# Optimization experiments

Hardware: AMD Instinct MI355X
Metric: run time of the kernel (lower is better)

The kernel has to match this reference:

```python
import jax, jax.numpy as jnp
import numpy as np

D_K = 128
SCALER = np.sqrt(D_K).astype(np.float32)

def setup_inputs() -> dict:
    key = jax.random.key(0)
    kq, kk, kv = jax.random.split(key, 3)
    B, L, D = 16, 2048, D_K
    q = jax.random.normal(kq, (B, L, D), dtype=jnp.float32)
    k = jax.random.normal(kk, (B, L, D), dtype=jnp.float32)
    v = jax.random.normal(kv, (B, L, D), dtype=jnp.float32)
    return {"q": q, "k": k, "v": v}

def reference(q, k, v):
    # score[b, i, j] = q[b, i, :] . k[b, j, :] / sqrt(d_k)
    score = jnp.einsum('bid,bjd->bij', q, k) / SCALER
    attn = jax.nn.softmax(score, axis=-1)
    # output[b, i, :] = sum_j attn[b, i, j] * v[b, j, :]
    return jnp.einsum('bij,bjd->bid', attn, v)
```

## Files before the change

kernel.cpp:

```cpp
#include <hip/hip_runtime.h>
#include <stdint.h>


typedef short bf16x8 __attribute__((ext_vector_type(8)));
typedef float f32x4 __attribute__((ext_vector_type(4)));
typedef float f32x16 __attribute__((ext_vector_type(16)));
typedef unsigned int u32;
typedef unsigned short u16;

#define L_SEQ  2048
#define D_HEAD 128
#define TSZ    8388608u
#define W_PART (2u * TSZ)
#define W_LSUM (W_PART + 768u * 32768u)
#define WS_NEED (W_LSUM + 768u * 128u * 4u)

__device__ __forceinline__ unsigned pk2(float lo, float hi) {
    union { float f; unsigned u; } a, b;
    a.f = lo; b.f = hi;
    return __builtin_amdgcn_perm(b.u + 0x8000u, a.u + 0x8000u, 0x07060302u);
}
__device__ __forceinline__ float ex2(float x) { return __builtin_amdgcn_exp2f(x); }
__device__ __forceinline__ float bflo(unsigned w) {
    union { unsigned u; float f; } v; v.u = w << 16; return v.f;
}
__device__ __forceinline__ float bfhi(unsigned w) {
    union { unsigned u; float f; } v; v.u = w & 0xffff0000u; return v.f;
}
__device__ __forceinline__ u32 cvtpk(float lo, float hi) {
    u32 d;
    asm("v_cvt_pk_bf16_f32 %0, %1, %2" : "=v"(d) : "v"(lo), "v"(hi));
    return d;
}
__device__ __forceinline__ void plswap(u32& a, u32& b) {
    asm volatile("v_permlane32_swap_b32 %0, %1" : "+v"(a), "+v"(b));
}
__device__ __forceinline__ void gl_lds16(const u16* g, u16* l) {
    __builtin_amdgcn_global_load_lds(
        (const __attribute__((address_space(1))) u32*)g,
        (__attribute__((address_space(3))) u32*)l, 16, 0, 0);
}

__global__ __launch_bounds__(256, 4)
void prepass(const float* __restrict__ K, const float* __restrict__ V,
             u16* __restrict__ kb, u16* __restrict__ vt) {
    const int id = blockIdx.x, t = threadIdx.x;
    if (id < 512) {
        const float* src = K + (size_t)id * 64 * 128;
        u16*        dst = kb + (size_t)id * 64 * 128;
        const int r = t >> 2;
        #pragma unroll
        for (int i = 0; i < 4; ++i) {
            int gp = (t & 3) * 4 + i;
            const float* s = src + r * 128 + gp * 8;
            float4 x0 = *(const float4*)s, x1 = *(const float4*)(s + 4);
            uint4 w;
            w.x = pk2(x0.x, x0.y); w.y = pk2(x0.z, x0.w);
            w.z = pk2(x1.x, x1.y); w.w = pk2(x1.z, x1.w);
            *(uint4*)(dst + (gp * 64 + r) * 8) = w;
        }
    } else {
        __shared__ __align__(16) u16 vl[128 * 72];
        const int bid = id - 512;
        const float* src = V + (size_t)bid * 64 * 128;
        const int vcc = t & 31, vgk = t >> 5;
        union { float4 v; float f[4]; } vr[8];
        const float* vp = src + (size_t)(vgk * 8) * 128 + vcc * 4;
        #pragma unroll
        for (int r = 0; r < 8; ++r) vr[r].v = *(const float4*)(vp + (size_t)r * 128);
        #pragma unroll
        for (int dd = 0; dd < 4; ++dd) {
            uint4 w;
            w.x = pk2(vr[0].f[dd], vr[1].f[dd]);
            w.y = pk2(vr[2].f[dd], vr[3].f[dd]);
            w.z = pk2(vr[4].f[dd], vr[5].f[dd]);
            w.w = pk2(vr[6].f[dd], vr[7].f[dd]);
            *(uint4*)(&vl[(vcc * 4 + dd) * 72 + vgk * 8]) = w;
        }
        __syncthreads();
        u16* dst = vt + (size_t)bid * 8192;
        #pragma unroll
        for (int i = 0; i < 4; ++i) {
            int c = i * 256 + t;
            int gv = c >> 7, d = c & 127;
            uint4 w = *(const uint4*)(&vl[d * 72 + gv * 8]);
            *(uint4*)(dst + (size_t)c * 8) = w;
        }
    }
}

__global__ __launch_bounds__(256, 2)
void attnR(const float* __restrict__ Qg, const u16* __restrict__ kb,
           const u16* __restrict__ vt, u16* __restrict__ part,
           float* __restrict__ lsum) {
    __shared__ __align__(16) char smem[32768];
    const int tid = threadIdx.x;
    const int qs = tid >> 6, lane = tid & 63;
    const int q32 = lane & 31, hi = lane >> 5;
    const int bid = blockIdx.x;
    const int kvh = bid >> 8, p = bid & 255;
    const int b = p & 15, qblk = p >> 4;
    const int t0 = kvh * 11;
    const int nt = (kvh < 2) ? 11 : 10;

    const float* Qp = Qg + (size_t)b * L_SEQ * D_HEAD;
    const u16*   Kp = kb + (size_t)b * L_SEQ * D_HEAD + (size_t)t0 * 8192;
    const u16*   Vp = vt + (size_t)b * 32 * 8192 + (size_t)t0 * 8192;
    u16* Kl = (u16*)smem;
    u16* Vl = (u16*)(smem + 16384);
    const int so = qs * 2048 + lane * 8;

    #pragma unroll
    for (int i = 0; i < 4; ++i) {
        gl_lds16(Kp + so + i * 512, Kl + so + i * 512);
        gl_lds16(Vp + so + i * 512, Vl + so + i * 512);
    }

    const float QS = 1.4426950408889634f / 11.313708498984761f;
    bf16x8 qf[8];
    {
        const float* qrow = Qp + (size_t)(qblk * 128 + qs * 32 + q32) * 128 + hi * 8;
        #pragma unroll
        for (int s8 = 0; s8 < 8; ++s8) {
            float4 x0 = *(const float4*)(qrow + s8 * 16);
            float4 x1 = *(const float4*)(qrow + s8 * 16 + 4);
            union { u32 u[4]; bf16x8 v; } tt;
            tt.u[0] = pk2(x0.x * QS, x0.y * QS);
            tt.u[1] = pk2(x0.z * QS, x0.w * QS);
            tt.u[2] = pk2(x1.x * QS, x1.y * QS);
            tt.u[3] = pk2(x1.z * QS, x1.w * QS);
            qf[s8] = tt.v;
        }
    }

    f32x16 acc[4];
    #pragma unroll
    for (int dt = 0; dt < 4; ++dt)
        acc[dt] = (f32x16){0.f,0.f,0.f,0.f,0.f,0.f,0.f,0.f,
                           0.f,0.f,0.f,0.f,0.f,0.f,0.f,0.f};
    float lrun = 0.f;

    __syncthreads();

    for (int it = 0; it < nt; ++it) {
        f32x16 st0 = (f32x16){0.f,0.f,0.f,0.f,0.f,0.f,0.f,0.f,
                              0.f,0.f,0.f,0.f,0.f,0.f,0.f,0.f};
        f32x16 st1 = st0;
        const u16* Kbase = Kl + hi * 512 + q32 * 8;
        #pragma unroll
        for (int s8 = 0; s8 < 8; ++s8) {
            bf16x8 a0 = *(const bf16x8*)(Kbase + s8 * 1024);
            bf16x8 a1 = *(const bf16x8*)(Kbase + s8 * 1024 + 256);
            st0 = __builtin_amdgcn_mfma_f32_32x32x16_bf16(a0, qf[s8], st0, 0, 0, 0);
            st1 = __builtin_amdgcn_mfma_f32_32x32x16_bf16(a1, qf[s8], st1, 0, 0, 0);
        }
        __syncthreads();

        if (it + 1 < nt) {
            const u16* kg = Kp + (size_t)(it + 1) * 8192 + so;
            #pragma unroll
            for (int i = 0; i < 4; ++i) gl_lds16(kg + i * 512, Kl + so + i * 512);
        }

        bf16x8 pf[4];
        #pragma unroll
        for (int v = 0; v < 2; ++v) {
            float pp[16];
            #pragma unroll
            for (int e = 0; e < 16; ++e) {
                float sv = (v == 0) ? st0[e] : st1[e];
                pp[e] = ex2(sv);
                lrun += pp[e];
            }
            u32 wa0 = cvtpk(pp[0], pp[1]),  wb0 = cvtpk(pp[4], pp[5]);
            u32 wa1 = cvtpk(pp[2], pp[3]),  wb1 = cvtpk(pp[6], pp[7]);
            plswap(wa0, wb0); plswap(wa1, wb1);
            u32 wc0 = cvtpk(pp[8], pp[9]),  wd0 = cvtpk(pp[12], pp[13]);
            u32 wc1 = cvtpk(pp[10], pp[11]), wd1 = cvtpk(pp[14], pp[15]);
            plswap(wc0, wd0); plswap(wc1, wd1);
            union { u32 u[4]; bf16x8 x; } t0u, t1u;
            t0u.u[0] = wa0; t0u.u[1] = wa1; t0u.u[2] = wb0; t0u.u[3] = wb1;
            t1u.u[0] = wc0; t1u.u[1] = wc1; t1u.u[2] = wd0; t1u.u[3] = wd1;
            pf[v * 2]     = t0u.x;
            pf[v * 2 + 1] = t1u.x;
        }

        const u16* Vbase = Vl + hi * 1024 + q32 * 8;
        #pragma unroll
        for (int dt = 0; dt < 4; ++dt) {
            #pragma unroll
            for (int ks = 0; ks < 4; ++ks) {
                bf16x8 av = *(const bf16x8*)(Vbase + ks * 2048 + dt * 256);
                acc[dt] = __builtin_amdgcn_mfma_f32_32x32x16_bf16(av, pf[ks], acc[dt], 0, 0, 0);
            }
        }
        __syncthreads();

        if (it + 1 < nt) {
            const u16* vg = Vp + (size_t)(it + 1) * 8192 + so;
            #pragma unroll
            for (int i = 0; i < 4; ++i) gl_lds16(vg + i * 512, Vl + so + i * 512);
        }
    }

    float l = lrun + __shfl_xor(lrun, 32);
    uint2* pw = (uint2*)(part + (size_t)bid * 16384);
    #pragma unroll
    for (int dt = 0; dt < 4; ++dt) {
        f32x16 o = acc[dt];
        #pragma unroll
        for (int jj = 0; jj < 4; ++jj) {
            uint2 w;
            w.x = pk2(o[jj * 4 + 0], o[jj * 4 + 1]);
            w.y = pk2(o[jj * 4 + 2], o[jj * 4 + 3]);
            pw[(((qs * 4 + dt) * 4 + jj) << 6) + lane] = w;
        }
    }
    if (lane < 32)
        lsum[(size_t)bid * 128 + qs * 32 + lane] = l;
}

__global__ __launch_bounds__(256, 2)
void combineR(const u16* __restrict__ part, const float* __restrict__ lsum,
              float* __restrict__ Og) {
    __shared__ float inv[128];
    __shared__ __align__(16) float Ol[64 * 132];
    const int t = threadIdx.x, p = blockIdx.x;
    const int b = p & 15, qblk = p >> 4;
    if (t < 128) {
        float l = lsum[(size_t)p * 128 + t]
                + lsum[(size_t)(256 + p) * 128 + t]
                + lsum[(size_t)(512 + p) * 128 + t];
        inv[t] = 1.0f / l;
    }
    const uint2* S0 = (const uint2*)(part + (size_t)p * 16384);
    const uint2* S1 = (const uint2*)(part + (size_t)(256 + p) * 16384);
    const uint2* S2 = (const uint2*)(part + (size_t)(512 + p) * 16384);
    __syncthreads();
    #pragma unroll
    for (int h = 0; h < 2; ++h) {
        #pragma unroll
        for (int i = 0; i < 8; ++i) {
            int slot = i * 256 + t;
            int qs_l = slot >> 10;
            int dt   = (slot >> 8) & 3;
            int jj   = (slot >> 6) & 3;
            int lane = slot & 63;
            int hi = lane >> 5, q32 = lane & 31;
            int qs = h * 2 + qs_l;
            int row_l = qs_l * 32 + q32;
            int d0 = dt * 32 + hi * 4 + jj * 8;
            size_t idx = (size_t)(((qs * 4 + dt) * 4 + jj) << 6) + lane;
            uint2 w0 = S0[idx], w1 = S1[idx], w2 = S2[idx];
            float iv = inv[h * 64 + row_l];
            float4 o;
            o.x = (bflo(w0.x) + bflo(w1.x) + bflo(w2.x)) * iv;
            o.y = (bfhi(w0.x) + bfhi(w1.x) + bfhi(w2.x)) * iv;
            o.z = (bflo(w0.y) + bflo(w1.y) + bflo(w2.y)) * iv;
            o.w = (bfhi(w0.y) + bfhi(w1.y) + bfhi(w2.y)) * iv;
            *(float4*)(&Ol[row_l * 132 + d0]) = o;
        }
        __syncthreads();
        #pragma unroll
        for (int i = 0; i < 8; ++i) {
            int slot = i * 256 + t;
            int row = slot >> 5, c4 = slot & 31;
            float4 val = *(const float4*)(&Ol[row * 132 + c4 * 4]);
            size_t q = (size_t)b * L_SEQ + qblk * 128 + h * 64 + row;
            *(float4*)(Og + q * D_HEAD + c4 * 4) = val;
        }
        __syncthreads();
    }
}

extern "C" void kernel_launch(void* const* d_in, const int* in_sizes, int n_in,
                              void* d_out, int out_size, void* d_ws, size_t ws_size,
                              hipStream_t stream) {
    const float* q = (const float*)d_in[0];
    const float* k = (const float*)d_in[1];
    const float* v = (const float*)d_in[2];
    float* out = (float*)d_out;
    u16* kb = (u16*)d_ws;
    u16* vt = (u16*)((char*)d_ws + TSZ);
    u16* part = (u16*)((char*)d_ws + W_PART);
    float* ls = (float*)((char*)d_ws + W_LSUM);
    prepass<<<dim3(1024), dim3(256), 0, stream>>>(k, v, kb, vt);
    attnR<<<dim3(768), dim3(256), 0, stream>>>(q, kb, vt, part, ls);
    combineR<<<dim3(256), dim3(256), 0, stream>>>(part, ls, out);
}
```

Before: 136.8 us.

## Drop split-KV partials and combine pass; each block handles full KV for 64 rows

The attention kernel no longer splits the key sequence into three chunks with bf16 partial outputs and a separate combine kernel. Each block of 128 threads now processes 64 query rows across all 32 KV tiles and writes normalized fp32 output directly. This removes the partial-write traffic, the combine launch and bf16 rounding of partials. In exchange there are fewer and longer blocks (512 blocks of 2 waves), and each block loads K/V tiles from global memory for only 64 rows, so there is less reuse per load and less overlap from waves sharing a tile.

Result: slower. 148.1 us (+8.3%).

```diff
diff --git a/kernel.cpp b/kernel.cpp
--- a/kernel.cpp
+++ b/kernel.cpp
@@ -3,7 +3,6 @@
 
 
 typedef short bf16x8 __attribute__((ext_vector_type(8)));
-typedef float f32x4 __attribute__((ext_vector_type(4)));
 typedef float f32x16 __attribute__((ext_vector_type(16)));
 typedef unsigned int u32;
 typedef unsigned short u16;
@@ -11,9 +10,6 @@
 #define L_SEQ  2048
 #define D_HEAD 128
 #define TSZ    8388608u
-#define W_PART (2u * TSZ)
-#define W_LSUM (W_PART + 768u * 32768u)
-#define WS_NEED (W_LSUM + 768u * 128u * 4u)
 
 __device__ __forceinline__ unsigned pk2(float lo, float hi) {
     union { float f; unsigned u; } a, b;
@@ -21,12 +17,6 @@
     return __builtin_amdgcn_perm(b.u + 0x8000u, a.u + 0x8000u, 0x07060302u);
 }
 __device__ __forceinline__ float ex2(float x) { return __builtin_amdgcn_exp2f(x); }
-__device__ __forceinline__ float bflo(unsigned w) {
-    union { unsigned u; float f; } v; v.u = w << 16; return v.f;
-}
-__device__ __forceinline__ float bfhi(unsigned w) {
-    union { unsigned u; float f; } v; v.u = w & 0xffff0000u; return v.f;
-}
 __device__ __forceinline__ u32 cvtpk(float lo, float hi) {
     u32 d;
     asm("v_cvt_pk_bf16_f32 %0, %1, %2" : "=v"(d) : "v"(lo), "v"(hi));
@@ -89,37 +79,34 @@
     }
 }
 
-__global__ __launch_bounds__(256, 2)
-void attnR(const float* __restrict__ Qg, const u16* __restrict__ kb,
-           const u16* __restrict__ vt, u16* __restrict__ part,
-           float* __restrict__ lsum) {
+__global__ __launch_bounds__(128, 2)
+void attnF(const float* __restrict__ Qg, const u16* __restrict__ kb,
+           const u16* __restrict__ vt, float* __restrict__ Og) {
     __shared__ __align__(16) char smem[32768];
     const int tid = threadIdx.x;
     const int qs = tid >> 6, lane = tid & 63;
     const int q32 = lane & 31, hi = lane >> 5;
-    const int bid = blockIdx.x;
-    const int kvh = bid >> 8, p = bid & 255;
+    const int p = blockIdx.x;
     const int b = p & 15, qblk = p >> 4;
-    const int t0 = kvh * 11;
-    const int nt = (kvh < 2) ? 11 : 10;
+    const int nt = 32;
 
     const float* Qp = Qg + (size_t)b * L_SEQ * D_HEAD;
-    const u16*   Kp = kb + (size_t)b * L_SEQ * D_HEAD + (size_t)t0 * 8192;
-    const u16*   Vp = vt + (size_t)b * 32 * 8192 + (size_t)t0 * 8192;
+    const u16*   Kp = kb + (size_t)b * L_SEQ * D_HEAD;
+    const u16*   Vp = vt + (size_t)b * 32 * 8192;
     u16* Kl = (u16*)smem;
     u16* Vl = (u16*)(smem + 16384);
-    const int so = qs * 2048 + lane * 8;
+    const int so = tid * 8;
 
     #pragma unroll
-    for (int i = 0; i < 4; ++i) {
-        gl_lds16(Kp + so + i * 512, Kl + so + i * 512);
-        gl_lds16(Vp + so + i * 512, Vl + so + i * 512);
+    for (int i = 0; i < 8; ++i) {
+        gl_lds16(Kp + so + i * 1024, Kl + so + i * 1024);
+        gl_lds16(Vp + so + i * 1024, Vl + so + i * 1024);
     }
 
     const float QS = 1.4426950408889634f / 11.313708498984761f;
     bf16x8 qf[8];
     {
-        const float* qrow = Qp + (size_t)(qblk * 128 + qs * 32 + q32) * 128 + hi * 8;
+        const float* qrow = Qp + (size_t)(qblk * 64 + qs * 32 + q32) * 128 + hi * 8;
         #pragma unroll
         for (int s8 = 0; s8 < 8; ++s8) {
             float4 x0 = *(const float4*)(qrow + s8 * 16);
@@ -159,7 +146,7 @@
         if (it + 1 < nt) {
             const u16* kg = Kp + (size_t)(it + 1) * 8192 + so;
             #pragma unroll
-            for (int i = 0; i < 4; ++i) gl_lds16(kg + i * 512, Kl + so + i * 512);
+            for (int i = 0; i < 8; ++i) gl_lds16(kg + i * 1024, Kl + so + i * 1024);
         }
 
         bf16x8 pf[4];
@@ -199,77 +186,24 @@
         if (it + 1 < nt) {
             const u16* vg = Vp + (size_t)(it + 1) * 8192 + so;
             #pragma unroll
-            for (int i = 0; i < 4; ++i) gl_lds16(vg + i * 512, Vl + so + i * 512);
+            for (int i = 0; i < 8; ++i) gl_lds16(vg + i * 1024, Vl + so + i * 1024);
         }
     }
 
     float l = lrun + __shfl_xor(lrun, 32);
-    uint2* pw = (uint2*)(part + (size_t)bid * 16384);
+    float iv = 1.0f / l;
+    float* orow = Og + ((size_t)b * L_SEQ + qblk * 64 + qs * 32 + q32) * 128;
     #pragma unroll
     for (int dt = 0; dt < 4; ++dt) {
-        f32x16 o = acc[dt];
         #pragma unroll
         for (int jj = 0; jj < 4; ++jj) {
-            uint2 w;
-            w.x = pk2(o[jj * 4 + 0], o[jj * 4 + 1]);
-            w.y = pk2(o[jj * 4 + 2], o[jj * 4 + 3]);
-            pw[(((qs * 4 + dt) * 4 + jj) << 6) + lane] = w;
-        }
-    }
-    if (lane < 32)
-        lsum[(size_t)bid * 128 + qs * 32 + lane] = l;
-}
-
-__global__ __launch_bounds__(256, 2)
-void combineR(const u16* __restrict__ part, const float* __restrict__ lsum,
-              float* __restrict__ Og) {
-    __shared__ float inv[128];
-    __shared__ __align__(16) float Ol[64 * 132];
-    const int t = threadIdx.x, p = blockIdx.x;
-    const int b = p & 15, qblk = p >> 4;
-    if (t < 128) {
-        float l = lsum[(size_t)p * 128 + t]
-                + lsum[(size_t)(256 + p) * 128 + t]
-                + lsum[(size_t)(512 + p) * 128 + t];
-        inv[t] = 1.0f / l;
-    }
-    const uint2* S0 = (const uint2*)(part + (size_t)p * 16384);
-    const uint2* S1 = (const uint2*)(part + (size_t)(256 + p) * 16384);
-    const uint2* S2 = (const uint2*)(part + (size_t)(512 + p) * 16384);
-    __syncthreads();
-    #pragma unroll
-    for (int h = 0; h < 2; ++h) {
-        #pragma unroll
-        for (int i = 0; i < 8; ++i) {
-            int slot = i * 256 + t;
-            int qs_l = slot >> 10;
-            int dt   = (slot >> 8) & 3;
-            int jj   = (slot >> 6) & 3;
-            int lane = slot & 63;
-            int hi = lane >> 5, q32 = lane & 31;
-            int qs = h * 2 + qs_l;
-            int row_l = qs_l * 32 + q32;
-            int d0 = dt * 32 + hi * 4 + jj * 8;
-            size_t idx = (size_t)(((qs * 4 + dt) * 4 + jj) << 6) + lane;
-            uint2 w0 = S0[idx], w1 = S1[idx], w2 = S2[idx];
-            float iv = inv[h * 64 + row_l];
-            float4 o;
-            o.x = (bflo(w0.x) + bflo(w1.x) + bflo(w2.x)) * iv;
-            o.y = (bfhi(w0.x) + bfhi(w1.x) + bfhi(w2.x)) * iv;
-            o.z = (bflo(w0.y) + bflo(w1.y) + bflo(w2.y)) * iv;
-            o.w = (bfhi(w0.y) + bfhi(w1.y) + bfhi(w2.y)) * iv;
-            *(float4*)(&Ol[row_l * 132 + d0]) = o;
-        }
-        __syncthreads();
-        #pragma unroll
-        for (int i = 0; i < 8; ++i) {
-            int slot = i * 256 + t;
-            int row = slot >> 5, c4 = slot & 31;
-            float4 val = *(const float4*)(&Ol[row * 132 + c4 * 4]);
-            size_t q = (size_t)b * L_SEQ + qblk * 128 + h * 64 + row;
-            *(float4*)(Og + q * D_HEAD + c4 * 4) = val;
-        }
-        __syncthreads();
+            float4 w;
+            w.x = acc[dt][jj * 4 + 0] * iv;
+            w.y = acc[dt][jj * 4 + 1] * iv;
+            w.z = acc[dt][jj * 4 + 2] * iv;
+            w.w = acc[dt][jj * 4 + 3] * iv;
+            *(float4*)(orow + dt * 32 + hi * 4 + jj * 8) = w;
+        }
     }
 }
 
@@ -282,9 +216,6 @@
     float* out = (float*)d_out;
     u16* kb = (u16*)d_ws;
     u16* vt = (u16*)((char*)d_ws + TSZ);
-    u16* part = (u16*)((char*)d_ws + W_PART);
-    float* ls = (float*)((char*)d_ws + W_LSUM);
     prepass<<<dim3(1024), dim3(256), 0, stream>>>(k, v, kb, vt);
-    attnR<<<dim3(768), dim3(256), 0, stream>>>(q, kb, vt, part, ls);
-    combineR<<<dim3(256), dim3(256), 0, stream>>>(part, ls, out);
-}
+    attnF<<<dim3(512), dim3(128), 0, stream>>>(q, kb, vt, out);
+}
```
